# Kernel tuning notes

Hardware: AMD Instinct MI355X
Metric: run time of the kernel (lower is better)

## Reference

```python
import jax, jax.numpy as jnp
import numpy as np
import math

B, S, D, H = 2, 2048, 1024, 16
HD = D // H  # 64 head features


def setup_inputs() -> dict:
    key = jax.random.key(0)
    ks = jax.random.split(key, 6)
    x = jax.random.normal(ks[0], (B, S, D), jnp.float32)
    wq = jax.random.normal(ks[1], (D, D), jnp.float32) * 0.02
    wk = jax.random.normal(ks[2], (D, D), jnp.float32) * 0.02
    wv = jax.random.normal(ks[3], (D, D), jnp.float32) * 0.02
    wo = jax.random.normal(ks[4], (D, D), jnp.float32) * 0.02
    # Llama-style RoPE frequencies: unit-modulus complex per (pos, pair),
    # stored as separate cos/sin arrays of shape [S, HD//2].
    inv_freq = 1.0 / (10000.0 ** (jnp.arange(0, HD, 2, dtype=jnp.float32) / HD))
    ang = jnp.arange(S, dtype=jnp.float32)[:, None] * inv_freq[None, :]
    freq_cos = jnp.cos(ang)
    freq_sin = jnp.sin(ang)
    # realistic padding: each sequence keeps a random prefix of at least S//2 tokens
    lengths = jax.random.randint(ks[5], (B,), S // 2, S + 1)
    padding_mask = (jnp.arange(S)[None, :] < lengths[:, None]).astype(jnp.int32)
    return dict(x=x, wq=wq, wk=wk, wv=wv, wo=wo,
                freq_cos=freq_cos, freq_sin=freq_sin, padding_mask=padding_mask)


def _apply_rope(t, cos, sin):
    # t: [B, S, H, HD]; cos/sin: [S, HD//2]
    tr = t.reshape(t.shape[:-1] + (HD // 2, 2))
    t0, t1 = tr[..., 0], tr[..., 1]
    c = cos[None, :, None, :]
    s = sin[None, :, None, :]
    o0 = t0 * c - t1 * s  # real part of complex multiply
    o1 = t0 * s + t1 * c  # imag part
    return jnp.stack([o0, o1], axis=-1).reshape(t.shape)


def reference(x, wq, wk, wv, wo, freq_cos, freq_sin, padding_mask):
    # QKV projections (torch Linear: y = x @ W.T, no bias)
    q = (x @ wq.T).reshape(B, S, H, HD)
    k = (x @ wk.T).reshape(B, S, H, HD)
    v = (x @ wv.T).reshape(B, S, H, HD)
    q = _apply_rope(q, freq_cos, freq_sin)
    k = _apply_rope(k, freq_cos, freq_sin)
    q = jnp.transpose(q, (0, 2, 1, 3))  # [B,H,S,HD]
    k = jnp.transpose(k, (0, 2, 1, 3))
    v = jnp.transpose(v, (0, 2, 1, 3))
    # NOTE: original scales by sqrt(n_features), not sqrt(head_dim)
    scores = jnp.einsum('bhqd,bhkd->bhqk', q, k) / math.sqrt(D)
    bias = jnp.where(padding_mask[:, None, None, :] == 0,
                     jnp.float32(-jnp.inf), jnp.float32(0.0))
    p = jax.nn.softmax(scores + bias, axis=-1)
    out = jnp.einsum('bhqk,bhkd->bhqd', p, v)
    out = jnp.transpose(out, (0, 2, 1, 3)).reshape(B, S, D)
    return out @ wo.T
```

## Files before the change

kernel.cpp:

```cpp
#include <hip/hip_runtime.h>
#include <hip/hip_bf16.h>
#include <stdint.h>

typedef unsigned short u16;
typedef __attribute__((ext_vector_type(8))) short bf16x8;
typedef __attribute__((ext_vector_type(4))) float f32x4;
typedef __attribute__((ext_vector_type(16))) float f32x16;

__device__ __forceinline__ u16 f2bf(float f) {
  union { float f; uint32_t u; } a; a.f = f;
  return (u16)((a.u + 0x7FFFu + ((a.u >> 16) & 1u)) >> 16);
}

__device__ __forceinline__ void gload_lds16(const void* g, void* l) {
  auto* gp = (__attribute__((address_space(1))) void*)(uintptr_t)g;
  auto* lp = (__attribute__((address_space(3))) void*)(uintptr_t)l;
  __builtin_amdgcn_global_load_lds(gp, lp, 16, 0, 0);
}

__device__ __forceinline__ float exp2_fast(float x) {
  float r;
  asm("v_exp_f32 %0, %1" : "=v"(r) : "v"(x));
  return r;
}

template <int N> __device__ __forceinline__ void waitvm() {
  if constexpr (N == 3)      asm volatile("s_waitcnt vmcnt(3)" ::: "memory");
  else if constexpr (N == 4) asm volatile("s_waitcnt vmcnt(4)" ::: "memory");
  else                       asm volatile("s_waitcnt vmcnt(0)" ::: "memory");
}

#define CVTPK(d, a, b) asm("v_cvt_pk_bf16_f32 %0, %1, %2" : "=v"(d) : "v"(a), "v"(b))
#define SWAP32(a, b)   asm("v_permlane32_swap_b32 %0, %1" : "+v"(a), "+v"(b))
#define BARRIER() do { asm volatile("" ::: "memory"); __builtin_amdgcn_s_barrier(); asm volatile("" ::: "memory"); } while (0)

__global__ void cvt_kernel(const float4* __restrict__ x, const float4* __restrict__ wq,
                           const float4* __restrict__ wk, const float4* __restrict__ wv,
                           const float4* __restrict__ wo,
                           ushort4* __restrict__ xb, ushort4* __restrict__ wqkv,
                           ushort4* __restrict__ wob) {
  const int XN = (2 * 2048 * 1024) / 4;
  const int WN = (1024 * 1024) / 4;
  const int total = XN + 4 * WN;
  for (int i = blockIdx.x * 256 + threadIdx.x; i < total; i += gridDim.x * 256) {
    float4 v; ushort4* dst;
    if (i < XN) { v = x[i]; dst = xb + i; }
    else {
      int j = i - XN; int m = j >> 18; int o = j & (WN - 1);
      const float4* src = (m == 0) ? wq : (m == 1) ? wk : (m == 2) ? wv : wo;
      v = src[o];
      dst = (m < 3) ? (wqkv + j) : (wob + o);
    }
    ushort4 r; r.x = f2bf(v.x); r.y = f2bf(v.y); r.z = f2bf(v.z); r.w = f2bf(v.w);
    *dst = r;
  }
}

__global__ void len_kernel(const int* __restrict__ mask, int* __restrict__ lens) {
  __shared__ int red[256];
  int b = blockIdx.x, s = 0;
  for (int i = threadIdx.x; i < 2048; i += 256) s += mask[b * 2048 + i];
  red[threadIdx.x] = s;
  __syncthreads();
  if (threadIdx.x < 64) {
    int v = red[threadIdx.x] + red[threadIdx.x + 64] + red[threadIdx.x + 128] + red[threadIdx.x + 192];
    #pragma unroll
    for (int o = 32; o > 0; o >>= 1) v += __shfl_down(v, o);
    if (threadIdx.x == 0) lens[b] = v;
  }
}

template <int BM, int BN, int MODE>
__global__ __launch_bounds__(256, 3)
void gemm3(const u16* __restrict__ A, const u16* __restrict__ Bm,
           int nTm, float* __restrict__ outf,
           u16* __restrict__ Qb, u16* __restrict__ Kb, u16* __restrict__ VbT,
           const float* __restrict__ cosT, const float* __restrict__ sinT) {
  constexpr int MREP = BM / 32;
  constexpr int NREP = BN / 32;
  constexpr int LA = BM / 64;
  constexpr int LB = BN / 64;
  constexpr int LOADS = LA + LB;
  __shared__ alignas(16) u16 SA[3][BM * 32];
  __shared__ alignas(16) u16 SB[3][BN * 32];

  const int tid = threadIdx.x, lane = tid & 63, wid = tid >> 6;
  const int wm = (wid >> 1) * (BM / 2), wn = (wid & 1) * (BN / 2);
  const int lr = lane & 15, lg = lane >> 4;

  const int cpx = gridDim.x >> 3;
  const int bid = (blockIdx.x & 7) * cpx + (blockIdx.x >> 3);
  const int m0 = (bid % nTm) * BM;
  const int n0 = (bid / nTm) * BN;

  const int srow = tid >> 2;
  const int schunk = (tid & 3) ^ ((srow >> 1) & 3);
  const u16* gA = A + (int64_t)(m0 + srow) * 1024 + schunk * 8;
  const u16* gB = Bm + (int64_t)(n0 + srow) * 1024 + schunk * 8;
  const int sdst = wid * 512;

#define STAGE(b, t) do { const int _ko = (t) * 32; \
    _Pragma("unroll") for (int j = 0; j < LA; ++j) \
      gload_lds16(gA + (int64_t)(j * 64) * 1024 + _ko, &SA[b][j * 2048 + sdst]); \
    _Pragma("unroll") for (int j = 0; j < LB; ++j) \
      gload_lds16(gB + (int64_t)(j * 64) * 1024 + _ko, &SB[b][j * 2048 + sdst]); } while (0)

  f32x4 acc[MREP][NREP];
  #pragma unroll
  for (int i = 0; i < MREP; ++i)
    #pragma unroll
    for (int j = 0; j < NREP; ++j)
      #pragma unroll
      for (int e = 0; e < 4; ++e) acc[i][j][e] = 0.0f;

  const int rchunk = (lg ^ ((lr >> 1) & 3)) * 8;

  STAGE(0, 0);
  STAGE(1, 1);
  waitvm<LOADS>();
  BARRIER();

  int bc = 0, bs = 2;
  for (int t = 0; t < 32; ++t) {
    if (t < 30) STAGE(bs, t + 2);
    const u16* sa = SA[bc];
    const u16* sb = SB[bc];
    bf16x8 af[MREP], bfm[NREP];
    #pragma unroll
    for (int i = 0; i < MREP; ++i) af[i] = *(const bf16x8*)&sa[(wm + i * 16 + lr) * 32 + rchunk];
    #pragma unroll
    for (int i = 0; i < NREP; ++i) bfm[i] = *(const bf16x8*)&sb[(wn + i * 16 + lr) * 32 + rchunk];
    #pragma unroll
    for (int mi = 0; mi < MREP; ++mi)
      #pragma unroll
      for (int ni = 0; ni < NREP; ++ni)
        acc[mi][ni] = __builtin_amdgcn_mfma_f32_16x16x32_bf16(af[mi], bfm[ni], acc[mi][ni], 0, 0, 0);
    if (t < 30) waitvm<LOADS>();
    else        waitvm<0>();
    BARRIER();
    bc = (bc == 2) ? 0 : bc + 1;
    bs = (bs == 2) ? 0 : bs + 1;
  }

  if (MODE == 0) {
    #pragma unroll
    for (int mi = 0; mi < MREP; ++mi)
      #pragma unroll
      for (int r = 0; r < 4; ++r) {
        const int row = m0 + wm + mi * 16 + lg * 4 + r;
        float* orow = outf + (int64_t)row * 1024 + n0 + wn + lr;
        #pragma unroll
        for (int ni = 0; ni < NREP; ++ni) orow[ni * 16] = acc[mi][ni][r];
      }
  } else {
    #pragma unroll
    for (int mi = 0; mi < MREP; ++mi) {
      #pragma unroll
      for (int r = 0; r < 4; ++r) {
        const int row = m0 + wm + mi * 16 + lg * 4 + r;
        const int bb = row >> 11, ss = row & 2047;
        #pragma unroll
        for (int ni = 0; ni < NREP; ++ni) {
          const int n = n0 + wn + ni * 16 + lr;
          float v = acc[mi][ni][r];
          if (n < 2048) {
            float partner = __shfl_xor(v, 1);
            const int ii = (n >> 1) & 31;
            const float c = cosT[ss * 32 + ii];
            const float sn = sinT[ss * 32 + ii];
            float rv = (n & 1) ? (partner * sn + v * c) : (v * c - partner * sn);
            const int h = (n >> 6) & 15, d = n & 63;
            const int idx = ((bb * 16 + h) * 2048 + ss) * 64 + d;
            if (n < 1024) Qb[idx] = f2bf(rv * 0.0450842298f);
            else          Kb[idx] = f2bf(rv);
          } else {
            const int n2 = n - 2048;
            const int h = n2 >> 6, d = n2 & 63;
            VbT[((int64_t)(bb * 16 + h) * 64 + d) * 2048 + ss] = f2bf(v);
          }
        }
      }
    }
  }
#undef STAGE
}

__global__ __launch_bounds__(256, 2)
void attn_kernel(const u16* __restrict__ Qb, const u16* __restrict__ Kb,
                 const u16* __restrict__ VbT, u16* __restrict__ attnb,
                 const int* __restrict__ lens) {
  __shared__ alignas(16) u16 Klds[2][2][64 * 64];
  __shared__ alignas(16) u16 Vlds[2][2][64 * 64];
  const int tid = threadIdx.x, lane = tid & 63, wid = tid >> 6;
  const int hi = lane >> 5, ql = lane & 31;
  const int bh = blockIdx.x >> 4;
  const int len = lens[bh >> 4];
  const int qrow = (blockIdx.x & 15) * 128 + wid * 32 + ql;

  bf16x8 qf[4];
  const u16* qptr = Qb + ((int64_t)bh * 2048 + qrow) * 64 + hi * 8;
  #pragma unroll
  for (int c = 0; c < 4; ++c) qf[c] = *(const bf16x8*)(qptr + c * 16);

  const int srow = tid >> 3, schunk = (tid & 7) ^ (srow & 7);
  const u16* kg = Kb + ((int64_t)bh * 2048 + srow) * 64 + schunk * 8;
  const u16* vg = VbT + ((int64_t)bh * 64 + srow) * 2048 + schunk * 8;
  const int dstoff = wid * 512;

#define ASTAGE(b, t) do { const int _k0 = (t) * 128; \
    _Pragma("unroll") for (int su = 0; su < 2; ++su) { \
      gload_lds16(kg + (int64_t)(_k0 + su * 64) * 64,        &Klds[b][su][dstoff]); \
      gload_lds16(kg + (int64_t)(_k0 + su * 64 + 32) * 64,   &Klds[b][su][2048 + dstoff]); \
      gload_lds16(vg + _k0 + su * 64,                        &Vlds[b][su][dstoff]); \
      gload_lds16(vg + _k0 + su * 64 + 32 * 2048,            &Vlds[b][su][2048 + dstoff]); } } while (0)

  f32x16 oacc[2];
  #pragma unroll
  for (int r = 0; r < 16; ++r) { oacc[0][r] = 0.0f; oacc[1][r] = 0.0f; }
  float mrun = -1e30f, lrun = 0.0f;

  const int nt = (len + 127) >> 7;
  ASTAGE(0, 0);
  __syncthreads();

  for (int t = 0; t < nt; ++t) {
    const int bu = t & 1;
    if (t + 1 < nt) ASTAGE(bu ^ 1, t + 1);

    f32x16 s[2][2];
    #pragma unroll
    for (int su = 0; su < 2; ++su)
      #pragma unroll
      for (int h = 0; h < 2; ++h)
        #pragma unroll
        for (int r = 0; r < 16; ++r) s[su][h][r] = 0.0f;
    __builtin_amdgcn_s_setprio(1);
    #pragma unroll
    for (int su = 0; su < 2; ++su)
      #pragma unroll
      for (int c = 0; c < 4; ++c) {
        const int slot = (((2 * c + hi) ^ (ql & 7)) * 8);
        bf16x8 kf0 = *(const bf16x8*)&Klds[bu][su][ql * 64 + slot];
        bf16x8 kf1 = *(const bf16x8*)&Klds[bu][su][(32 + ql) * 64 + slot];
        s[su][0] = __builtin_amdgcn_mfma_f32_32x32x16_bf16(kf0, qf[c], s[su][0], 0, 0, 0);
        s[su][1] = __builtin_amdgcn_mfma_f32_32x32x16_bf16(kf1, qf[c], s[su][1], 0, 0, 0);
      }
    __builtin_amdgcn_s_setprio(0);

    const int k0 = t * 128;
    if (k0 + 128 > len) {
      #pragma unroll
      for (int su = 0; su < 2; ++su)
        #pragma unroll
        for (int r = 0; r < 16; ++r) {
          const int key = k0 + su * 64 + (r & 3) + 8 * (r >> 2) + 4 * hi;
          if (key >= len)      s[su][0][r] = -1e30f;
          if (key + 32 >= len) s[su][1][r] = -1e30f;
        }
    }

    float ma = -1e30f, mb = -1e30f, mc = -1e30f, md = -1e30f;
    #pragma unroll
    for (int su = 0; su < 2; ++su)
      #pragma unroll
      for (int h = 0; h < 2; ++h)
        #pragma unroll
        for (int r = 0; r < 16; r += 4) {
          ma = fmaxf(ma, s[su][h][r]);
          mb = fmaxf(mb, s[su][h][r + 1]);
          mc = fmaxf(mc, s[su][h][r + 2]);
          md = fmaxf(md, s[su][h][r + 3]);
        }
    float mx = fmaxf(fmaxf(ma, mb), fmaxf(mc, md));
    mx = fmaxf(mx, __shfl_xor(mx, 32));
    if (!__all(mx - mrun <= 11.0f)) {
      const float mnew = fmaxf(mrun, mx);
      const float sc = exp2_fast(mrun - mnew);
      #pragma unroll
      for (int r = 0; r < 16; ++r) { oacc[0][r] *= sc; oacc[1][r] *= sc; }
      lrun *= sc;
      mrun = mnew;
    }

    float ps0 = 0.0f, ps1 = 0.0f;
    bf16x8 pfrag[8];
    #pragma unroll
    for (int su = 0; su < 2; ++su) {
      float p0[16], p1[16];
      #pragma unroll
      for (int r = 0; r < 16; r += 2) {
        p0[r]     = exp2_fast(s[su][0][r] - mrun);
        p0[r + 1] = exp2_fast(s[su][0][r + 1] - mrun);
        p1[r]     = exp2_fast(s[su][1][r] - mrun);
        p1[r + 1] = exp2_fast(s[su][1][r + 1] - mrun);
        ps0 += p0[r] + p1[r];
        ps1 += p0[r + 1] + p1[r + 1];
      }
      #pragma unroll
      for (int ks = 0; ks < 4; ++ks) {
        const float* pp = (ks < 2) ? p0 : p1;
        const int o = (ks & 1) * 8;
        uint32_t a0, a1, a2, a3;
        CVTPK(a0, pp[o + 0], pp[o + 1]);
        CVTPK(a1, pp[o + 2], pp[o + 3]);
        CVTPK(a2, pp[o + 4], pp[o + 5]);
        CVTPK(a3, pp[o + 6], pp[o + 7]);
        SWAP32(a0, a2);
        SWAP32(a1, a3);
        union { uint32_t u[4]; bf16x8 v; } pw;
        pw.u[0] = a0; pw.u[1] = a1; pw.u[2] = a2; pw.u[3] = a3;
        pfrag[su * 4 + ks] = pw.v;
      }
    }
    float psum = ps0 + ps1;
    psum += __shfl_xor(psum, 32);
    lrun += psum;

    __builtin_amdgcn_s_setprio(1);
    #pragma unroll
    for (int dc = 0; dc < 2; ++dc) {
      const int drow = dc * 32 + ql;
      #pragma unroll
      for (int su = 0; su < 2; ++su)
        #pragma unroll
        for (int ks = 0; ks < 4; ++ks) {
          const int slot = (((2 * ks + hi) ^ (ql & 7)) * 8);
          bf16x8 vf = *(const bf16x8*)&Vlds[bu][su][drow * 64 + slot];
          oacc[dc] = __builtin_amdgcn_mfma_f32_32x32x16_bf16(vf, pfrag[su * 4 + ks], oacc[dc], 0, 0, 0);
        }
    }
    __builtin_amdgcn_s_setprio(0);
    __syncthreads();
  }
#undef ASTAGE

  const float inv = 1.0f / lrun;
  u16* outp = attnb + ((int64_t)((bh >> 4) * 2048 + qrow)) * 1024 + (bh & 15) * 64;
  #pragma unroll
  for (int dc = 0; dc < 2; ++dc)
    #pragma unroll
    for (int g = 0; g < 4; ++g) {
      ushort4 w;
      w.x = f2bf(oacc[dc][4 * g + 0] * inv);
      w.y = f2bf(oacc[dc][4 * g + 1] * inv);
      w.z = f2bf(oacc[dc][4 * g + 2] * inv);
      w.w = f2bf(oacc[dc][4 * g + 3] * inv);
      *(ushort4*)(outp + dc * 32 + 8 * g + 4 * hi) = w;
    }
}

extern "C" void kernel_launch(void* const* d_in, const int* in_sizes, int n_in,
                              void* d_out, int out_size, void* d_ws, size_t ws_size,
                              hipStream_t stream) {
  const float* x    = (const float*)d_in[0];
  const float* wq   = (const float*)d_in[1];
  const float* wk   = (const float*)d_in[2];
  const float* wv   = (const float*)d_in[3];
  const float* wo   = (const float*)d_in[4];
  const float* fcos = (const float*)d_in[5];
  const float* fsin = (const float*)d_in[6];
  const int*   pmsk = (const int*)d_in[7];
  float* out = (float*)d_out;

  char* ws = (char*)d_ws;
  u16* XB    = (u16*)(ws);
  u16* WQKV  = (u16*)(ws + (size_t)8  * 1048576);
  u16* WOB   = (u16*)(ws + (size_t)14 * 1048576);
  u16* QB    = (u16*)(ws + (size_t)16 * 1048576);
  u16* KB    = (u16*)(ws + (size_t)24 * 1048576);
  u16* VBT   = (u16*)(ws + (size_t)32 * 1048576);
  u16* ATTNB = (u16*)(ws + (size_t)40 * 1048576);
  int* LENS  = (int*)(ws + (size_t)48 * 1048576);

  cvt_kernel<<<2048, 256, 0, stream>>>((const float4*)x, (const float4*)wq,
                                       (const float4*)wk, (const float4*)wv,
                                       (const float4*)wo, (ushort4*)XB,
                                       (ushort4*)WQKV, (ushort4*)WOB);
  len_kernel<<<2, 256, 0, stream>>>(pmsk, LENS);

  gemm3<128, 128, 1><<<768, 256, 0, stream>>>(XB, WQKV, 32, nullptr,
                                              QB, KB, VBT, fcos, fsin);

  attn_kernel<<<512, 256, 0, stream>>>(QB, KB, VBT, ATTNB, LENS);

  gemm3<128, 64, 0><<<512, 256, 0, stream>>>(ATTNB, WOB, 32, out,
                                             nullptr, nullptr, nullptr, nullptr, nullptr);
}
```

Before: 120.2 us.

## Replace QKV GEMM with 256x256-tile 8-wave ping-pong kernel

Adds a new QKV projection kernel that uses 256x256 output tiles, 512 threads and 128KB of dynamic LDS with XOR-swizzled layout. The K loop is split into quadrant MFMA phases interleaved with async global-to-LDS loads, and uses s_setprio around the MFMAs. Blocks are remapped across XCDs. This is meant to raise data reuse per block and overlap loads with compute, at the cost of only 192 blocks (fewer than 256 CUs) and heavy LDS/register use. The RoPE/scatter epilogue moves from gemm3 MODE 1 into the new kernel.

```diff
diff --git a/kernel.cpp b/kernel.cpp
--- a/kernel.cpp
+++ b/kernel.cpp
@@ -70,6 +70,129 @@
   }
 }
 
+__global__ __launch_bounds__(512, 2)
+void gemm8p(const u16* __restrict__ A, const u16* __restrict__ Bm, int nTm,
+            u16* __restrict__ Qb, u16* __restrict__ Kb, u16* __restrict__ VbT,
+            const float* __restrict__ cosT, const float* __restrict__ sinT) {
+  extern __shared__ __align__(16) u16 lds[];
+  u16* SAm = lds;
+  u16* SBm = lds + 32768;
+  const int tid = threadIdx.x, lane = tid & 63, wid = tid >> 6;
+  const int wm = wid >> 2, wn = wid & 3;
+  const int lr = lane & 15, lg = lane >> 4;
+
+  const int cpx = gridDim.x >> 3;
+  const int bid = (blockIdx.x & 7) * cpx + (blockIdx.x >> 3);
+  const int m0 = (bid % nTm) * 256;
+  const int n0 = (bid / nTm) * 256;
+
+  const int srow = tid >> 3;
+  const int schunk = (tid & 7) ^ ((srow >> 1) & 7);
+  const u16* gA = A + (int64_t)(m0 + srow) * 1024 + schunk * 8;
+  const u16* gB = Bm + (int64_t)(n0 + (srow & 31) + (srow >> 5) * 64) * 1024 + schunk * 8;
+  const int ldst = wid * 512;
+
+#define SA_STAGE(buf, h, kt) do { \
+    gload_lds16(gA + (int64_t)((h) * 64) * 1024 + (kt) * 64,         &SAm[(buf) * 16384 + (h) * 8192 + ldst]); \
+    gload_lds16(gA + (int64_t)((h) * 64 + 128) * 1024 + (kt) * 64,   &SAm[(buf) * 16384 + (h) * 8192 + 4096 + ldst]); } while (0)
+#define SB_STAGE(buf, nh, kt) do { \
+    gload_lds16(gB + (int64_t)((nh) * 32) * 1024 + (kt) * 64,        &SBm[(buf) * 16384 + (nh) * 8192 + ldst]); \
+    gload_lds16(gB + (int64_t)((nh) * 32 + 128) * 1024 + (kt) * 64,  &SBm[(buf) * 16384 + (nh) * 8192 + 4096 + ldst]); } while (0)
+#define RD_AF(buf, mh, dst) do { \
+    _Pragma("unroll") for (int miL = 0; miL < 4; ++miL) { \
+      const int rloc = miL * 16 + lr + wm * 64; \
+      _Pragma("unroll") for (int ks = 0; ks < 2; ++ks) \
+        dst[miL][ks] = *(const bf16x8*)&SAm[(buf) * 16384 + (mh) * 8192 + rloc * 64 + (((ks * 4 + lg) ^ ((rloc >> 1) & 7)) * 8)]; } } while (0)
+#define RD_BF(buf, nh, dst) do { \
+    _Pragma("unroll") for (int nfL = 0; nfL < 2; ++nfL) { \
+      const int rloc = nfL * 16 + lr + wn * 32; \
+      _Pragma("unroll") for (int ks = 0; ks < 2; ++ks) \
+        dst[nfL][ks] = *(const bf16x8*)&SBm[(buf) * 16384 + (nh) * 8192 + rloc * 64 + (((ks * 4 + lg) ^ ((rloc >> 1) & 7)) * 8)]; } } while (0)
+#define QUAD(mh, nh, af, bf) do { \
+    __builtin_amdgcn_s_setprio(1); \
+    _Pragma("unroll") for (int ks = 0; ks < 2; ++ks) \
+    _Pragma("unroll") for (int miL = 0; miL < 4; ++miL) \
+    _Pragma("unroll") for (int nfL = 0; nfL < 2; ++nfL) \
+      acc[(mh) * 4 + miL][(nh) * 2 + nfL] = __builtin_amdgcn_mfma_f32_16x16x32_bf16( \
+          af[miL][ks], bf[nfL][ks], acc[(mh) * 4 + miL][(nh) * 2 + nfL], 0, 0, 0); \
+    __builtin_amdgcn_s_setprio(0); } while (0)
+
+  f32x4 acc[8][4];
+  #pragma unroll
+  for (int i = 0; i < 8; ++i)
+    #pragma unroll
+    for (int j = 0; j < 4; ++j)
+      #pragma unroll
+      for (int e = 0; e < 4; ++e) acc[i][j][e] = 0.0f;
+
+  SA_STAGE(0, 0, 0); SB_STAGE(0, 1, 0); SA_STAGE(0, 1, 0); SB_STAGE(0, 0, 0);
+  SA_STAGE(1, 0, 1); SB_STAGE(1, 1, 1);
+  waitvm<4>();
+  BARRIER();
+
+  bf16x8 afA[4][2], afB[4][2], bf0[2][2], bf1[2][2];
+  for (int u = 0; u < 8; ++u) {
+    const int k2 = 2 * u;
+    const bool pf = (u < 7);
+    RD_AF(0, 0, afA); RD_BF(0, 0, bf0);
+    SA_STAGE(1, 1, k2 + 1);
+    BARRIER(); QUAD(0, 0, afA, bf0); BARRIER();
+    RD_BF(0, 1, bf1);
+    SB_STAGE(1, 0, k2 + 1);
+    BARRIER(); QUAD(0, 1, afA, bf1); BARRIER();
+    RD_AF(0, 1, afB);
+    if (pf) SA_STAGE(0, 0, k2 + 2);
+    BARRIER(); QUAD(1, 1, afB, bf1); BARRIER();
+    if (pf) { SB_STAGE(0, 1, k2 + 2); waitvm<4>(); } else { waitvm<0>(); }
+    BARRIER(); QUAD(1, 0, afB, bf0); BARRIER();
+    RD_AF(1, 0, afA); RD_BF(1, 0, bf0);
+    if (pf) SA_STAGE(0, 1, k2 + 2);
+    BARRIER(); QUAD(0, 0, afA, bf0); BARRIER();
+    RD_BF(1, 1, bf1);
+    if (pf) SB_STAGE(0, 0, k2 + 2);
+    BARRIER(); QUAD(0, 1, afA, bf1); BARRIER();
+    RD_AF(1, 1, afB);
+    if (pf) SA_STAGE(1, 0, k2 + 3);
+    BARRIER(); QUAD(1, 1, afB, bf1); BARRIER();
+    if (pf) { SB_STAGE(1, 1, k2 + 3); waitvm<4>(); } else { waitvm<0>(); }
+    BARRIER(); QUAD(1, 0, afB, bf0); BARRIER();
+  }
+
+  #pragma unroll
+  for (int mi = 0; mi < 8; ++mi) {
+    #pragma unroll
+    for (int r = 0; r < 4; ++r) {
+      const int row = m0 + wm * 128 + mi * 16 + lg * 4 + r;
+      const int bb = row >> 11, ss = row & 2047;
+      #pragma unroll
+      for (int nf = 0; nf < 4; ++nf) {
+        const int n = n0 + wn * 64 + nf * 16 + lr;
+        float v = acc[mi][nf][r];
+        if (n < 2048) {
+          float partner = __shfl_xor(v, 1);
+          const int ii = (n >> 1) & 31;
+          const float c = cosT[ss * 32 + ii];
+          const float sn = sinT[ss * 32 + ii];
+          float rv = (n & 1) ? (partner * sn + v * c) : (v * c - partner * sn);
+          const int h = (n >> 6) & 15, d = n & 63;
+          const int idx = ((bb * 16 + h) * 2048 + ss) * 64 + d;
+          if (n < 1024) Qb[idx] = f2bf(rv * 0.0450842298f);
+          else          Kb[idx] = f2bf(rv);
+        } else {
+          const int n2 = n - 2048;
+          const int h = n2 >> 6, d = n2 & 63;
+          VbT[((int64_t)(bb * 16 + h) * 64 + d) * 2048 + ss] = f2bf(v);
+        }
+      }
+    }
+  }
+#undef SA_STAGE
+#undef SB_STAGE
+#undef RD_AF
+#undef RD_BF
+#undef QUAD
+}
+
 template <int BM, int BN, int MODE>
 __global__ __launch_bounds__(256, 3)
 void gemm3(const u16* __restrict__ A, const u16* __restrict__ Bm,
@@ -152,35 +275,6 @@
         #pragma unroll
         for (int ni = 0; ni < NREP; ++ni) orow[ni * 16] = acc[mi][ni][r];
       }
-  } else {
-    #pragma unroll
-    for (int mi = 0; mi < MREP; ++mi) {
-      #pragma unroll
-      for (int r = 0; r < 4; ++r) {
-        const int row = m0 + wm + mi * 16 + lg * 4 + r;
-        const int bb = row >> 11, ss = row & 2047;
-        #pragma unroll
-        for (int ni = 0; ni < NREP; ++ni) {
-          const int n = n0 + wn + ni * 16 + lr;
-          float v = acc[mi][ni][r];
-          if (n < 2048) {
-            float partner = __shfl_xor(v, 1);
-            const int ii = (n >> 1) & 31;
-            const float c = cosT[ss * 32 + ii];
-            const float sn = sinT[ss * 32 + ii];
-            float rv = (n & 1) ? (partner * sn + v * c) : (v * c - partner * sn);
-            const int h = (n >> 6) & 15, d = n & 63;
-            const int idx = ((bb * 16 + h) * 2048 + ss) * 64 + d;
-            if (n < 1024) Qb[idx] = f2bf(rv * 0.0450842298f);
-            else          Kb[idx] = f2bf(rv);
-          } else {
-            const int n2 = n - 2048;
-            const int h = n2 >> 6, d = n2 & 63;
-            VbT[((int64_t)(bb * 16 + h) * 64 + d) * 2048 + ss] = f2bf(v);
-          }
-        }
-      }
-    }
   }
 #undef STAGE
 }
@@ -372,14 +466,16 @@
   u16* ATTNB = (u16*)(ws + (size_t)40 * 1048576);
   int* LENS  = (int*)(ws + (size_t)48 * 1048576);
 
+  hipFuncSetAttribute((const void*)gemm8p,
+                      hipFuncAttributeMaxDynamicSharedMemorySize, 131072);
+
   cvt_kernel<<<2048, 256, 0, stream>>>((const float4*)x, (const float4*)wq,
                                        (const float4*)wk, (const float4*)wv,
                                        (const float4*)wo, (ushort4*)XB,
                                        (ushort4*)WQKV, (ushort4*)WOB);
   len_kernel<<<2, 256, 0, stream>>>(pmsk, LENS);
 
-  gemm3<128, 128, 1><<<768, 256, 0, stream>>>(XB, WQKV, 32, nullptr,
-                                              QB, KB, VBT, fcos, fsin);
+  gemm8p<<<192, 512, 131072, stream>>>(XB, WQKV, 16, QB, KB, VBT, fcos, fsin);
 
   attn_kernel<<<512, 256, 0, stream>>>(QB, KB, VBT, ATTNB, LENS);
 
```

After: 123.5 us. 1.03x slower.

## Switch GEMMs to 64-wide K tiles with double buffering

Applied to the files above, without the earlier changes.

Both projection GEMMs now stage 64-element K slices, with an 8-chunk XOR swizzle, into two LDS buffers instead of 32-element slices into three buffers. The loop runs 16 iterations with two MFMA k-steps each, which halves the number of barriers and wait points. In exchange the prefetch depth drops to one stage and every iteration waits on vmcnt(0), so load latency may be less well hidden. LDS use per block grows from 48KB to 64KB, which may limit occupancy below the 3 blocks per CU the launch bounds ask for.

```diff
diff --git a/kernel.cpp b/kernel.cpp
--- a/kernel.cpp
+++ b/kernel.cpp
@@ -24,15 +24,10 @@
   return r;
 }
 
-template <int N> __device__ __forceinline__ void waitvm() {
-  if constexpr (N == 3)      asm volatile("s_waitcnt vmcnt(3)" ::: "memory");
-  else if constexpr (N == 4) asm volatile("s_waitcnt vmcnt(4)" ::: "memory");
-  else                       asm volatile("s_waitcnt vmcnt(0)" ::: "memory");
-}
-
 #define CVTPK(d, a, b) asm("v_cvt_pk_bf16_f32 %0, %1, %2" : "=v"(d) : "v"(a), "v"(b))
 #define SWAP32(a, b)   asm("v_permlane32_swap_b32 %0, %1" : "+v"(a), "+v"(b))
 #define BARRIER() do { asm volatile("" ::: "memory"); __builtin_amdgcn_s_barrier(); asm volatile("" ::: "memory"); } while (0)
+#define WAITVM0() asm volatile("s_waitcnt vmcnt(0)" ::: "memory")
 
 __global__ void cvt_kernel(const float4* __restrict__ x, const float4* __restrict__ wq,
                            const float4* __restrict__ wk, const float4* __restrict__ wv,
@@ -72,17 +67,16 @@
 
 template <int BM, int BN, int MODE>
 __global__ __launch_bounds__(256, 3)
-void gemm3(const u16* __restrict__ A, const u16* __restrict__ Bm,
-           int nTm, float* __restrict__ outf,
-           u16* __restrict__ Qb, u16* __restrict__ Kb, u16* __restrict__ VbT,
-           const float* __restrict__ cosT, const float* __restrict__ sinT) {
+void gemm64(const u16* __restrict__ A, const u16* __restrict__ Bm,
+            int nTm, float* __restrict__ outf,
+            u16* __restrict__ Qb, u16* __restrict__ Kb, u16* __restrict__ VbT,
+            const float* __restrict__ cosT, const float* __restrict__ sinT) {
   constexpr int MREP = BM / 32;
   constexpr int NREP = BN / 32;
-  constexpr int LA = BM / 64;
-  constexpr int LB = BN / 64;
-  constexpr int LOADS = LA + LB;
-  __shared__ alignas(16) u16 SA[3][BM * 32];
-  __shared__ alignas(16) u16 SB[3][BN * 32];
+  constexpr int LA = BM / 32;
+  constexpr int LB = BN / 32;
+  __shared__ alignas(16) u16 SA[2][BM * 64];
+  __shared__ alignas(16) u16 SB[2][BN * 64];
 
   const int tid = threadIdx.x, lane = tid & 63, wid = tid >> 6;
   const int wm = (wid >> 1) * (BM / 2), wn = (wid & 1) * (BN / 2);
@@ -93,17 +87,17 @@
   const int m0 = (bid % nTm) * BM;
   const int n0 = (bid / nTm) * BN;
 
-  const int srow = tid >> 2;
-  const int schunk = (tid & 3) ^ ((srow >> 1) & 3);
+  const int srow = tid >> 3;
+  const int schunk = (tid & 7) ^ ((srow >> 1) & 7);
   const u16* gA = A + (int64_t)(m0 + srow) * 1024 + schunk * 8;
   const u16* gB = Bm + (int64_t)(n0 + srow) * 1024 + schunk * 8;
   const int sdst = wid * 512;
 
-#define STAGE(b, t) do { const int _ko = (t) * 32; \
+#define STAGE(b, t) do { const int _ko = (t) * 64; \
     _Pragma("unroll") for (int j = 0; j < LA; ++j) \
-      gload_lds16(gA + (int64_t)(j * 64) * 1024 + _ko, &SA[b][j * 2048 + sdst]); \
+      gload_lds16(gA + (int64_t)(j * 32) * 1024 + _ko, &SA[b][j * 2048 + sdst]); \
     _Pragma("unroll") for (int j = 0; j < LB; ++j) \
-      gload_lds16(gB + (int64_t)(j * 64) * 1024 + _ko, &SB[b][j * 2048 + sdst]); } while (0)
+      gload_lds16(gB + (int64_t)(j * 32) * 1024 + _ko, &SB[b][j * 2048 + sdst]); } while (0)
 
   f32x4 acc[MREP][NREP];
   #pragma unroll
@@ -113,33 +107,39 @@
       #pragma unroll
       for (int e = 0; e < 4; ++e) acc[i][j][e] = 0.0f;
 
-  const int rchunk = (lg ^ ((lr >> 1) & 3)) * 8;
-
   STAGE(0, 0);
-  STAGE(1, 1);
-  waitvm<LOADS>();
+  WAITVM0();
   BARRIER();
 
-  int bc = 0, bs = 2;
-  for (int t = 0; t < 32; ++t) {
-    if (t < 30) STAGE(bs, t + 2);
-    const u16* sa = SA[bc];
-    const u16* sb = SB[bc];
-    bf16x8 af[MREP], bfm[NREP];
-    #pragma unroll
-    for (int i = 0; i < MREP; ++i) af[i] = *(const bf16x8*)&sa[(wm + i * 16 + lr) * 32 + rchunk];
-    #pragma unroll
-    for (int i = 0; i < NREP; ++i) bfm[i] = *(const bf16x8*)&sb[(wn + i * 16 + lr) * 32 + rchunk];
-    #pragma unroll
-    for (int mi = 0; mi < MREP; ++mi)
-      #pragma unroll
-      for (int ni = 0; ni < NREP; ++ni)
-        acc[mi][ni] = __builtin_amdgcn_mfma_f32_16x16x32_bf16(af[mi], bfm[ni], acc[mi][ni], 0, 0, 0);
-    if (t < 30) waitvm<LOADS>();
-    else        waitvm<0>();
+  for (int t = 0; t < 16; ++t) {
+    const int bu = t & 1;
+    if (t < 15) STAGE(bu ^ 1, t + 1);
+    const u16* sa = SA[bu];
+    const u16* sb = SB[bu];
+    bf16x8 af[MREP][2], bfm[NREP][2];
+    #pragma unroll
+    for (int i = 0; i < MREP; ++i) {
+      const int row = wm + i * 16 + lr;
+      #pragma unroll
+      for (int ks = 0; ks < 2; ++ks)
+        af[i][ks] = *(const bf16x8*)&sa[row * 64 + (((ks * 4 + lg) ^ ((row >> 1) & 7)) * 8)];
+    }
+    #pragma unroll
+    for (int i = 0; i < NREP; ++i) {
+      const int row = wn + i * 16 + lr;
+      #pragma unroll
+      for (int ks = 0; ks < 2; ++ks)
+        bfm[i][ks] = *(const bf16x8*)&sb[row * 64 + (((ks * 4 + lg) ^ ((row >> 1) & 7)) * 8)];
+    }
+    #pragma unroll
+    for (int ks = 0; ks < 2; ++ks)
+      #pragma unroll
+      for (int mi = 0; mi < MREP; ++mi)
+        #pragma unroll
+        for (int ni = 0; ni < NREP; ++ni)
+          acc[mi][ni] = __builtin_amdgcn_mfma_f32_16x16x32_bf16(af[mi][ks], bfm[ni][ks], acc[mi][ni], 0, 0, 0);
+    WAITVM0();
     BARRIER();
-    bc = (bc == 2) ? 0 : bc + 1;
-    bs = (bs == 2) ? 0 : bs + 1;
   }
 
   if (MODE == 0) {
@@ -378,11 +378,11 @@
                                        (ushort4*)WQKV, (ushort4*)WOB);
   len_kernel<<<2, 256, 0, stream>>>(pmsk, LENS);
 
-  gemm3<128, 128, 1><<<768, 256, 0, stream>>>(XB, WQKV, 32, nullptr,
-                                              QB, KB, VBT, fcos, fsin);
+  gemm64<128, 128, 1><<<768, 256, 0, stream>>>(XB, WQKV, 32, nullptr,
+                                               QB, KB, VBT, fcos, fsin);
 
   attn_kernel<<<512, 256, 0, stream>>>(QB, KB, VBT, ATTNB, LENS);
 
-  gemm3<128, 64, 0><<<512, 256, 0, stream>>>(ATTNB, WOB, 32, out,
-                                             nullptr, nullptr, nullptr, nullptr, nullptr);
-}
+  gemm64<128, 64, 0><<<512, 256, 0, stream>>>(ATTNB, WOB, 32, out,
+                                              nullptr, nullptr, nullptr, nullptr, nullptr);
+}
```

Measured after the change: 129.5 us. 7.7% more time.

## Replace QKV GEMM with 256x256-tile 8-wave kernel and fold length reduction into cvt

Applied to the files above, without the earlier changes.

The QKV projection GEMM moves from 128x128 tiles on 256-thread blocks with a triple-buffered K=32 pipeline to 256x256 tiles on 512-thread blocks. The new kernel double-buffers K=64 stages in 128KB of dynamic LDS with an XOR swizzle, raises MFMA priority with s_setprio, and remaps block IDs across XCDs. It launches 192 blocks at one block per CU, which aims for more data reuse per LDS load but leaves some CUs idle and has no overlap between blocks. The padding-length reduction also moves into two extra blocks of the conversion kernel, removing one launch.

```diff
diff --git a/kernel.cpp b/kernel.cpp
--- a/kernel.cpp
+++ b/kernel.cpp
@@ -33,16 +33,32 @@
 #define CVTPK(d, a, b) asm("v_cvt_pk_bf16_f32 %0, %1, %2" : "=v"(d) : "v"(a), "v"(b))
 #define SWAP32(a, b)   asm("v_permlane32_swap_b32 %0, %1" : "+v"(a), "+v"(b))
 #define BARRIER() do { asm volatile("" ::: "memory"); __builtin_amdgcn_s_barrier(); asm volatile("" ::: "memory"); } while (0)
+#define WAITVM0() asm volatile("s_waitcnt vmcnt(0)" ::: "memory")
 
 __global__ void cvt_kernel(const float4* __restrict__ x, const float4* __restrict__ wq,
                            const float4* __restrict__ wk, const float4* __restrict__ wv,
                            const float4* __restrict__ wo,
                            ushort4* __restrict__ xb, ushort4* __restrict__ wqkv,
-                           ushort4* __restrict__ wob) {
+                           ushort4* __restrict__ wob,
+                           const int* __restrict__ mask, int* __restrict__ lens) {
+  if (blockIdx.x >= 2048) {
+    __shared__ int red[256];
+    int b = blockIdx.x - 2048, s = 0;
+    for (int i = threadIdx.x; i < 2048; i += 256) s += mask[b * 2048 + i];
+    red[threadIdx.x] = s;
+    __syncthreads();
+    if (threadIdx.x < 64) {
+      int v = red[threadIdx.x] + red[threadIdx.x + 64] + red[threadIdx.x + 128] + red[threadIdx.x + 192];
+      #pragma unroll
+      for (int o = 32; o > 0; o >>= 1) v += __shfl_down(v, o);
+      if (threadIdx.x == 0) lens[b] = v;
+    }
+    return;
+  }
   const int XN = (2 * 2048 * 1024) / 4;
   const int WN = (1024 * 1024) / 4;
   const int total = XN + 4 * WN;
-  for (int i = blockIdx.x * 256 + threadIdx.x; i < total; i += gridDim.x * 256) {
+  for (int i = blockIdx.x * 256 + threadIdx.x; i < total; i += 2048 * 256) {
     float4 v; ushort4* dst;
     if (i < XN) { v = x[i]; dst = xb + i; }
     else {
@@ -56,18 +72,105 @@
   }
 }
 
-__global__ void len_kernel(const int* __restrict__ mask, int* __restrict__ lens) {
-  __shared__ int red[256];
-  int b = blockIdx.x, s = 0;
-  for (int i = threadIdx.x; i < 2048; i += 256) s += mask[b * 2048 + i];
-  red[threadIdx.x] = s;
-  __syncthreads();
-  if (threadIdx.x < 64) {
-    int v = red[threadIdx.x] + red[threadIdx.x + 64] + red[threadIdx.x + 128] + red[threadIdx.x + 192];
-    #pragma unroll
-    for (int o = 32; o > 0; o >>= 1) v += __shfl_down(v, o);
-    if (threadIdx.x == 0) lens[b] = v;
-  }
+__global__ __launch_bounds__(512, 1)
+void gemm2ph(const u16* __restrict__ A, const u16* __restrict__ Bm, int nTm,
+             u16* __restrict__ Qb, u16* __restrict__ Kb, u16* __restrict__ VbT,
+             const float* __restrict__ cosT, const float* __restrict__ sinT) {
+  extern __shared__ __align__(16) u16 lds[];
+  u16* SA = lds;
+  u16* SB = lds + 32768;
+  const int tid = threadIdx.x, lane = tid & 63, wid = tid >> 6;
+  const int wm = (wid >> 2) * 128, wn = (wid & 3) * 64;
+  const int lr = lane & 15, lg = lane >> 4;
+
+  const int cpx = gridDim.x >> 3;
+  const int bid = (blockIdx.x & 7) * cpx + (blockIdx.x >> 3);
+  const int m0 = (bid % nTm) * 256;
+  const int n0 = (bid / nTm) * 256;
+
+  const int srow = tid >> 3;
+  const int schunk = (tid & 7) ^ ((srow >> 1) & 7);
+  const u16* gA = A + (int64_t)(m0 + srow) * 1024 + schunk * 8;
+  const u16* gB = Bm + (int64_t)(n0 + srow) * 1024 + schunk * 8;
+  const int sdst = wid * 512;
+
+#define STG(buf, t) do { const int _ko = (t) * 64; \
+    _Pragma("unroll") for (int j = 0; j < 4; ++j) \
+      gload_lds16(gA + (int64_t)(j * 64) * 1024 + _ko, &SA[(buf) * 16384 + j * 4096 + sdst]); \
+    _Pragma("unroll") for (int j = 0; j < 4; ++j) \
+      gload_lds16(gB + (int64_t)(j * 64) * 1024 + _ko, &SB[(buf) * 16384 + j * 4096 + sdst]); } while (0)
+
+  f32x4 acc[8][4];
+  #pragma unroll
+  for (int i = 0; i < 8; ++i)
+    #pragma unroll
+    for (int j = 0; j < 4; ++j)
+      #pragma unroll
+      for (int e = 0; e < 4; ++e) acc[i][j][e] = 0.0f;
+
+  STG(0, 0);
+  WAITVM0();
+  BARRIER();
+
+  for (int t = 0; t < 16; ++t) {
+    const int bu = t & 1;
+    if (t < 15) STG(bu ^ 1, t + 1);
+    const u16* sa = &SA[bu * 16384];
+    const u16* sb = &SB[bu * 16384];
+    #pragma unroll
+    for (int ks = 0; ks < 2; ++ks) {
+      bf16x8 af[8], bfm[4];
+      #pragma unroll
+      for (int mi = 0; mi < 8; ++mi) {
+        const int row = wm + mi * 16 + lr;
+        af[mi] = *(const bf16x8*)&sa[row * 64 + (((ks * 4 + lg) ^ ((row >> 1) & 7)) * 8)];
+      }
+      #pragma unroll
+      for (int ni = 0; ni < 4; ++ni) {
+        const int row = wn + ni * 16 + lr;
+        bfm[ni] = *(const bf16x8*)&sb[row * 64 + (((ks * 4 + lg) ^ ((row >> 1) & 7)) * 8)];
+      }
+      __builtin_amdgcn_s_setprio(1);
+      #pragma unroll
+      for (int mi = 0; mi < 8; ++mi)
+        #pragma unroll
+        for (int ni = 0; ni < 4; ++ni)
+          acc[mi][ni] = __builtin_amdgcn_mfma_f32_16x16x32_bf16(af[mi], bfm[ni], acc[mi][ni], 0, 0, 0);
+      __builtin_amdgcn_s_setprio(0);
+    }
+    WAITVM0();
+    BARRIER();
+  }
+
+  #pragma unroll
+  for (int mi = 0; mi < 8; ++mi) {
+    #pragma unroll
+    for (int r = 0; r < 4; ++r) {
+      const int row = m0 + wm + mi * 16 + lg * 4 + r;
+      const int bb = row >> 11, ss = row & 2047;
+      #pragma unroll
+      for (int ni = 0; ni < 4; ++ni) {
+        const int n = n0 + wn + ni * 16 + lr;
+        float v = acc[mi][ni][r];
+        if (n < 2048) {
+          float partner = __shfl_xor(v, 1);
+          const int ii = (n >> 1) & 31;
+          const float c = cosT[ss * 32 + ii];
+          const float sn = sinT[ss * 32 + ii];
+          float rv = (n & 1) ? (partner * sn + v * c) : (v * c - partner * sn);
+          const int h = (n >> 6) & 15, d = n & 63;
+          const int idx = ((bb * 16 + h) * 2048 + ss) * 64 + d;
+          if (n < 1024) Qb[idx] = f2bf(rv * 0.0450842298f);
+          else          Kb[idx] = f2bf(rv);
+        } else {
+          const int n2 = n - 2048;
+          const int h = n2 >> 6, d = n2 & 63;
+          VbT[((int64_t)(bb * 16 + h) * 64 + d) * 2048 + ss] = f2bf(v);
+        }
+      }
+    }
+  }
+#undef STG
 }
 
 template <int BM, int BN, int MODE>
@@ -152,35 +255,6 @@
         #pragma unroll
         for (int ni = 0; ni < NREP; ++ni) orow[ni * 16] = acc[mi][ni][r];
       }
-  } else {
-    #pragma unroll
-    for (int mi = 0; mi < MREP; ++mi) {
-      #pragma unroll
-      for (int r = 0; r < 4; ++r) {
-        const int row = m0 + wm + mi * 16 + lg * 4 + r;
-        const int bb = row >> 11, ss = row & 2047;
-        #pragma unroll
-        for (int ni = 0; ni < NREP; ++ni) {
-          const int n = n0 + wn + ni * 16 + lr;
-          float v = acc[mi][ni][r];
-          if (n < 2048) {
-            float partner = __shfl_xor(v, 1);
-            const int ii = (n >> 1) & 31;
-            const float c = cosT[ss * 32 + ii];
-            const float sn = sinT[ss * 32 + ii];
-            float rv = (n & 1) ? (partner * sn + v * c) : (v * c - partner * sn);
-            const int h = (n >> 6) & 15, d = n & 63;
-            const int idx = ((bb * 16 + h) * 2048 + ss) * 64 + d;
-            if (n < 1024) Qb[idx] = f2bf(rv * 0.0450842298f);
-            else          Kb[idx] = f2bf(rv);
-          } else {
-            const int n2 = n - 2048;
-            const int h = n2 >> 6, d = n2 & 63;
-            VbT[((int64_t)(bb * 16 + h) * 64 + d) * 2048 + ss] = f2bf(v);
-          }
-        }
-      }
-    }
   }
 #undef STAGE
 }
@@ -372,14 +446,15 @@
   u16* ATTNB = (u16*)(ws + (size_t)40 * 1048576);
   int* LENS  = (int*)(ws + (size_t)48 * 1048576);
 
-  cvt_kernel<<<2048, 256, 0, stream>>>((const float4*)x, (const float4*)wq,
+  hipFuncSetAttribute((const void*)gemm2ph,
+                      hipFuncAttributeMaxDynamicSharedMemorySize, 131072);
+
+  cvt_kernel<<<2050, 256, 0, stream>>>((const float4*)x, (const float4*)wq,
                                        (const float4*)wk, (const float4*)wv,
                                        (const float4*)wo, (ushort4*)XB,
-                                       (ushort4*)WQKV, (ushort4*)WOB);
-  len_kernel<<<2, 256, 0, stream>>>(pmsk, LENS);
-
-  gemm3<128, 128, 1><<<768, 256, 0, stream>>>(XB, WQKV, 32, nullptr,
-                                              QB, KB, VBT, fcos, fsin);
+                                       (ushort4*)WQKV, (ushort4*)WOB, pmsk, LENS);
+
+  gemm2ph<<<192, 512, 131072, stream>>>(XB, WQKV, 16, QB, KB, VBT, fcos, fsin);
 
   attn_kernel<<<512, 256, 0, stream>>>(QB, KB, VBT, ATTNB, LENS);
 
```

After: 122.9 us. +2.2%, slower.
